# Optimization experiments

Hardware: AMD Instinct MI355X
Metric: run time of the kernel (lower is better)

Reference implementation:

```python
import jax, jax.numpy as jnp
import numpy as np

BS, NQ, NK = 4096, 21, 7   # batch, num_neg queries, 7 keys (weekdays)
E = 512                     # key_size == query_size
H = 512                     # hidden_size
NEG_INF = -1e9


def setup_inputs() -> dict:
    key = jax.random.key(0)
    ks = jax.random.split(key, 6)
    sq = 1.0 / np.sqrt(E)
    sh = 1.0 / np.sqrt(H)
    return {
        "queries": jax.random.normal(ks[0], (BS, NQ, E), jnp.float32),
        "keys": jax.random.normal(ks[1], (BS, NK, E), jnp.float32),
        "wq_w": jax.random.normal(ks[2], (H, E), jnp.float32) * sq,
        "wq_b": jnp.zeros((H,), jnp.float32),
        "wk_w": jax.random.normal(ks[3], (H, E), jnp.float32) * sq,
        "wk_b": jnp.zeros((H,), jnp.float32),
        "wv_w": jax.random.normal(ks[4], (1, H), jnp.float32) * sh,
        "wv_b": jnp.zeros((1,), jnp.float32),
        "cum_subs_masks": jax.random.randint(ks[5], (BS, 1, NK, 1), 0, 2).astype(jnp.int32),
        "num_neg": NQ,
    }


def reference(queries, keys, wq_w, wq_b, wk_w, wk_b, wv_w, wv_b, cum_subs_masks, num_neg):
    # dropout p=0.0 -> identity (as in eval / p=0)
    q = jnp.einsum('bqe,he->bqh', queries, wq_w) + wq_b          # (bs,21,H)
    k = jnp.einsum('bke,he->bkh', keys, wk_w) + wk_b             # (bs,7,H)
    # additive score: broadcast q over keys, k over queries
    t = jnp.tanh(q[:, :, None, :] + k[:, None, :, :])            # (bs,21,7,H)
    scores = jnp.einsum('bqkh,oh->bqko', t, wv_w) + wv_b         # (bs,21,7,1)
    scores = scores + cum_subs_masks.astype(scores.dtype) * NEG_INF
    attn_weights = jax.nn.softmax(scores, axis=-2)               # softmax over 7 keys
    # weighted sum of the RAW keys (the module multiplies by expanded `keys`)
    attn_out = jnp.einsum('bqk,bke->bqe', attn_weights[..., 0], keys)  # (bs,21,E)
    return (attn_out, attn_weights)
```

## Files before the change

kernel.cpp:

```cpp
#include <hip/hip_runtime.h>
#include <hip/hip_bf16.h>

#define BS_   4096
#define NQ_   21
#define NK_   7
#define E_    512
#define MQ_   (BS_*NQ_)
#define MK_   (BS_*NK_)
#define MT1_  (MQ_/128)
#define MT2_  (MK_/128)
#define SCALE_ 2.88539008177792681f

typedef __attribute__((ext_vector_type(8))) short bf16x8;
typedef __attribute__((ext_vector_type(4))) float f32x4;
typedef __attribute__((ext_vector_type(8))) unsigned short u16x8;

__device__ __forceinline__ unsigned int cvt_pk_bf16(float lo, float hi){
  unsigned int r;
  asm("v_cvt_pk_bf16_f32 %0, %1, %2" : "=v"(r) : "v"(lo), "v"(hi));
  return r;
}
__device__ __forceinline__ float bf2f(unsigned short h){
  return __builtin_bit_cast(float, (unsigned int)h << 16);
}
__device__ __forceinline__ void gload_lds16(const void* g, void* l){
  __builtin_amdgcn_global_load_lds(
      (const __attribute__((address_space(1))) unsigned int*)g,
      (__attribute__((address_space(3))) unsigned int*)l, 16, 0, 0);
}

__global__ __launch_bounds__(256) void cast_weights(
    const float* __restrict__ wq, const float* __restrict__ wk,
    unsigned int* __restrict__ oq, unsigned int* __restrict__ ok)
{
  int i = blockIdx.x * 256 + threadIdx.x;
  float4 a = ((const float4*)wq)[i];
  float4 b = ((const float4*)wk)[i];
  uint2 ua = { cvt_pk_bf16(a.x, a.y), cvt_pk_bf16(a.z, a.w) };
  uint2 ub = { cvt_pk_bf16(b.x, b.y), cvt_pk_bf16(b.z, b.w) };
  ((uint2*)oq)[i] = ua;
  ((uint2*)ok)[i] = ub;
}

__global__ __launch_bounds__(256, 4)
void gemm_proj(const float* __restrict__ Aq, const float* __restrict__ Ak,
               const unsigned short* __restrict__ Bq, const unsigned short* __restrict__ Bk,
               const float* __restrict__ bq, const float* __restrict__ bk,
               unsigned short* __restrict__ Cq, unsigned short* __restrict__ Ck)
{
  __shared__ char Asm[2][128 * 64];
  __shared__ char Bsm[2][128 * 64];

  const int tid  = threadIdx.x;
  const int lane = tid & 63;
  const int w    = tid >> 6;
  const int wr   = w >> 1, wc = w & 1;

  const int orig = (int)blockIdx.x;
  const int j    = orig >> 3;
  int       mt   = (j >> 2) * 8 + (orig & 7);
  const int nt   = j & 3;

  const float* A; const unsigned short* Bw; const float* bias; unsigned short* C;
  if (mt < MT1_){ A = Aq; Bw = Bq; bias = bq; C = Cq; }
  else          { A = Ak; Bw = Bk; bias = bk; C = Ck; mt -= MT1_; }

  const long m0 = (long)mt << 7;
  const int  n0 = nt << 7;
  const char* Abyte = (const char*)(A + m0 * E_);
  const char* Bbyte = (const char*)Bw;

  long asrc[4]; int adst[4];
#pragma unroll
  for (int i = 0; i < 4; ++i){
    const int c   = tid + i * 256;
    const int row = c >> 3;
    const int sl  = c & 7;
    asrc[i] = (long)row * (E_ * 4) + sl * 16;
    adst[i] = row * 64 + (((sl & 6) * 8) ^ (((row >> 1) & 3) << 4)) + (sl & 1) * 8;
  }
  long bsrc[2]; int bdst[2];
#pragma unroll
  for (int i = 0; i < 2; ++i){
    const int c   = tid + i * 256;
    const int row = c >> 2;
    const int sl  = c & 3;
    bsrc[i] = (long)(n0 + row) * (E_ * 2) + ((sl * 16) ^ (((row >> 1) & 3) << 4));
    bdst[i] = c * 16;
  }

  int aoff[4], boff[4];
#pragma unroll
  for (int m = 0; m < 4; ++m){
    const int r = wr * 64 + m * 16 + (lane & 15);
    aoff[m] = r * 64 + ((16 * (lane >> 4)) ^ (((r >> 1) & 3) << 4));
  }
#pragma unroll
  for (int n = 0; n < 4; ++n){
    const int r = wc * 64 + n * 16 + (lane & 15);
    boff[n] = r * 64 + ((16 * (lane >> 4)) ^ (((r >> 1) & 3) << 4));
  }

  f32x4 acc[4][4];
  const f32x4 z4 = {0.f, 0.f, 0.f, 0.f};
#pragma unroll
  for (int m = 0; m < 4; ++m)
#pragma unroll
    for (int n = 0; n < 4; ++n) acc[m][n] = z4;

  {
    float4 av[4];
#pragma unroll
    for (int i = 0; i < 4; ++i) av[i] = *(const float4*)(Abyte + asrc[i]);
#pragma unroll
    for (int i = 0; i < 2; ++i) gload_lds16(Bbyte + bsrc[i], Bsm[0] + bdst[i]);
#pragma unroll
    for (int i = 0; i < 4; ++i){
      uint2 u = { cvt_pk_bf16(av[i].x, av[i].y), cvt_pk_bf16(av[i].z, av[i].w) };
      *(uint2*)(Asm[0] + adst[i]) = u;
    }
  }
  __syncthreads();

#pragma unroll 2
  for (int t = 0; t < 16; ++t){
    const int buf = t & 1, nbuf = buf ^ 1;
    float4 av[4];
    if (t < 15){
      const long ka = (long)(t + 1) * 128;
      const long kb = (long)(t + 1) * 64;
#pragma unroll
      for (int i = 0; i < 4; ++i) av[i] = *(const float4*)(Abyte + asrc[i] + ka);
#pragma unroll
      for (int i = 0; i < 2; ++i) gload_lds16(Bbyte + bsrc[i] + kb, Bsm[nbuf] + bdst[i]);
    }
    bf16x8 af[4], bfr[4];
#pragma unroll
    for (int m = 0; m < 4; ++m) af[m]  = *(const bf16x8*)(Asm[buf] + aoff[m]);
#pragma unroll
    for (int n = 0; n < 4; ++n) bfr[n] = *(const bf16x8*)(Bsm[buf] + boff[n]);
#pragma unroll
    for (int m = 0; m < 4; ++m)
#pragma unroll
      for (int n = 0; n < 4; ++n)
        acc[m][n] = __builtin_amdgcn_mfma_f32_16x16x32_bf16(af[m], bfr[n], acc[m][n], 0, 0, 0);
    if (t < 15){
#pragma unroll
      for (int i = 0; i < 4; ++i){
        uint2 u = { cvt_pk_bf16(av[i].x, av[i].y), cvt_pk_bf16(av[i].z, av[i].w) };
        *(uint2*)(Asm[nbuf] + adst[i]) = u;
      }
    }
    __syncthreads();
  }

  const int ccol0 = n0 + wc * 64 + (lane & 15);
  float bvs[4];
#pragma unroll
  for (int n = 0; n < 4; ++n) bvs[n] = bias[ccol0 + n * 16] * SCALE_;
#pragma unroll
  for (int m = 0; m < 4; ++m){
    const long rbase = m0 + wr * 64 + m * 16 + (lane >> 4) * 4;
#pragma unroll
    for (int n = 0; n < 4; ++n){
      const long col = ccol0 + n * 16;
      float v0 = fmaf(acc[m][n][0], SCALE_, bvs[n]);
      float v1 = fmaf(acc[m][n][1], SCALE_, bvs[n]);
      float v2 = fmaf(acc[m][n][2], SCALE_, bvs[n]);
      float v3 = fmaf(acc[m][n][3], SCALE_, bvs[n]);
      unsigned int u01 = cvt_pk_bf16(v0, v1);
      unsigned int u23 = cvt_pk_bf16(v2, v3);
      C[(rbase + 0) * E_ + col] = (unsigned short)(u01 & 0xffffu);
      C[(rbase + 1) * E_ + col] = (unsigned short)(u01 >> 16);
      C[(rbase + 2) * E_ + col] = (unsigned short)(u23 & 0xffffu);
      C[(rbase + 3) * E_ + col] = (unsigned short)(u23 >> 16);
    }
  }
}

__global__ __launch_bounds__(256, 2)
void attn_fused(const unsigned short* __restrict__ qp,
                const unsigned short* __restrict__ kp,
                const float* __restrict__ keys,
                const float* __restrict__ wv, const float* __restrict__ wvb,
                const int* __restrict__ mask,
                float* __restrict__ out0, float* __restrict__ out1)
{
  const int lane = threadIdx.x & 63;
  const int b    = blockIdx.x * 4 + (threadIdx.x >> 6);

  float wvr[8];
  *(float4*)&wvr[0] = ((const float4*)wv)[lane * 2];
  *(float4*)&wvr[4] = ((const float4*)wv)[lane * 2 + 1];

  float kf[NK_][8];
#pragma unroll
  for (int k = 0; k < NK_; ++k){
    u16x8 u = *(const u16x8*)(kp + ((long)b * NK_ + k) * E_ + lane * 8);
#pragma unroll
    for (int j = 0; j < 8; ++j) kf[k][j] = bf2f((unsigned short)u[j]);
  }
  float kr[NK_][8];
#pragma unroll
  for (int k = 0; k < NK_; ++k){
    const float4* p = (const float4*)(keys + ((long)b * NK_ + k) * E_ + lane * 8);
    *(float4*)&kr[k][0] = p[0];
    *(float4*)&kr[k][4] = p[1];
  }

  float wsum = ((wvr[0] + wvr[1]) + (wvr[2] + wvr[3])) + ((wvr[4] + wvr[5]) + (wvr[6] + wvr[7]));
#pragma unroll
  for (int off = 32; off; off >>= 1) wsum += __shfl_xor(wsum, off, 64);

  const float vb = wvb[0];
  float base[NK_];
#pragma unroll
  for (int k = 0; k < NK_; ++k)
    base[k] = (wsum + vb) + (float)mask[b * NK_ + k] * (-1e9f);

  const unsigned short* qrow = qp + (long)b * NQ_ * E_ + lane * 8;
  u16x8 qv = *(const u16x8*)qrow;

  float4* o0 = (float4*)(out0 + (long)b * NQ_ * E_) + lane * 2;
  float*  o1 = out1 + (long)b * (NQ_ * NK_);

  for (int qi = 0; qi < NQ_; ++qi){
    u16x8 qn = qv;
    if (qi < NQ_ - 1) qn = *(const u16x8*)(qrow + (qi + 1) * E_);

    float qf[8];
#pragma unroll
    for (int j = 0; j < 8; ++j) qf[j] = bf2f((unsigned short)qv[j]);
    qv = qn;

    float acc[NK_];
#pragma unroll
    for (int k = 0; k < NK_; ++k){
      float a = 0.f;
#pragma unroll
      for (int j = 0; j < 8; ++j){
        float x = qf[j] + kf[k][j];
        float e = __builtin_amdgcn_exp2f(x);
        float r = __builtin_amdgcn_rcpf(e + 1.0f);
        a = fmaf(wvr[j], r, a);
      }
      acc[k] = a;
    }
#pragma unroll
    for (int k = 0; k < NK_; ++k){
      float a = acc[k];
#pragma unroll
      for (int off = 32; off; off >>= 1) a += __shfl_xor(a, off, 64);
      acc[k] = a;
    }
    float sc[NK_], mx = -3.4e38f;
#pragma unroll
    for (int k = 0; k < NK_; ++k){ sc[k] = fmaf(-2.f, acc[k], base[k]); mx = fmaxf(mx, sc[k]); }
    float sum = 0.f;
#pragma unroll
    for (int k = 0; k < NK_; ++k){ sc[k] = __expf(sc[k] - mx); sum += sc[k]; }
    const float inv = __builtin_amdgcn_rcpf(sum);
    float wgt[NK_];
#pragma unroll
    for (int k = 0; k < NK_; ++k) wgt[k] = sc[k] * inv;

    float wsel = wgt[0];
#pragma unroll
    for (int k = 1; k < NK_; ++k) wsel = (lane == k) ? wgt[k] : wsel;
    if (lane < NK_) o1[qi * NK_ + lane] = wsel;

    float4 lo = {0.f,0.f,0.f,0.f}, hi = {0.f,0.f,0.f,0.f};
#pragma unroll
    for (int k = 0; k < NK_; ++k){
      lo.x = fmaf(wgt[k], kr[k][0], lo.x);
      lo.y = fmaf(wgt[k], kr[k][1], lo.y);
      lo.z = fmaf(wgt[k], kr[k][2], lo.z);
      lo.w = fmaf(wgt[k], kr[k][3], lo.w);
      hi.x = fmaf(wgt[k], kr[k][4], hi.x);
      hi.y = fmaf(wgt[k], kr[k][5], hi.y);
      hi.z = fmaf(wgt[k], kr[k][6], hi.z);
      hi.w = fmaf(wgt[k], kr[k][7], hi.w);
    }
    o0[qi * 128 + 0] = lo;
    o0[qi * 128 + 1] = hi;
  }
}

extern "C" void kernel_launch(void* const* d_in, const int* in_sizes, int n_in,
                              void* d_out, int out_size, void* d_ws, size_t ws_size,
                              hipStream_t stream)
{
  const float* queries = (const float*)d_in[0];
  const float* keys    = (const float*)d_in[1];
  const float* wq_w    = (const float*)d_in[2];
  const float* wq_b    = (const float*)d_in[3];
  const float* wk_w    = (const float*)d_in[4];
  const float* wk_b    = (const float*)d_in[5];
  const float* wv_w    = (const float*)d_in[6];
  const float* wv_b    = (const float*)d_in[7];
  const int*   mask    = (const int*)d_in[8];
  (void)in_sizes; (void)n_in; (void)out_size; (void)ws_size;

  float* out0 = (float*)d_out;
  float* out1 = out0 + (long)MQ_ * E_;

  char* ws = (char*)d_ws;
  unsigned short* wqb = (unsigned short*)ws;
  unsigned short* wkb = (unsigned short*)(ws + 512 * 512 * 2);
  unsigned short* qb  = (unsigned short*)(ws + (1 << 20));
  unsigned short* kb  = qb + (size_t)MQ_ * E_;

  cast_weights<<<dim3(256), dim3(256), 0, stream>>>(wq_w, wk_w, (unsigned int*)wqb, (unsigned int*)wkb);
  gemm_proj<<<dim3((MT1_ + MT2_) * 4), dim3(256), 0, stream>>>(
      queries, keys, wqb, wkb, wq_b, wk_b, qb, kb);
  attn_fused<<<dim3(BS_ / 4), dim3(256), 0, stream>>>(qb, kb, keys, wv_w, wv_b, mask, out0, out1);
}
```

Before: 251.6 us.

## Triple-buffer projection GEMM with two-stage-ahead prefetch and explicit waitcnts

Rewrites the projection GEMM main loop from a double-buffered scheme to a three-buffer pipeline that keeps loads for two K-steps in flight. It uses hand-placed s_waitcnt and raw barriers so global loads overlap with MFMA work across iterations. The loop is fully unrolled and the occupancy hint in launch_bounds is dropped. The extra LDS (48KB) and the extra register-held A tile may lower occupancy, and the manual waitcnt counts are fragile if the compiler reorders memory ops.

```diff
diff --git a/kernel.cpp b/kernel.cpp
--- a/kernel.cpp
+++ b/kernel.cpp
@@ -42,14 +42,14 @@
   ((uint2*)ok)[i] = ub;
 }
 
-__global__ __launch_bounds__(256, 4)
+__global__ __launch_bounds__(256)
 void gemm_proj(const float* __restrict__ Aq, const float* __restrict__ Ak,
                const unsigned short* __restrict__ Bq, const unsigned short* __restrict__ Bk,
                const float* __restrict__ bq, const float* __restrict__ bk,
                unsigned short* __restrict__ Cq, unsigned short* __restrict__ Ck)
 {
-  __shared__ char Asm[2][128 * 64];
-  __shared__ char Bsm[2][128 * 64];
+  __shared__ char Asm[3][128 * 64];
+  __shared__ char Bsm[3][128 * 64];
 
   const int tid  = threadIdx.x;
   const int lane = tid & 63;
@@ -108,51 +108,74 @@
 #pragma unroll
     for (int n = 0; n < 4; ++n) acc[m][n] = z4;
 
+#define STAGE_LOADS(av, T) do { \
+  _Pragma("unroll") for (int i_ = 0; i_ < 4; ++i_) \
+    av[i_] = *(const float4*)(Abyte + asrc[i_] + (long)(T) * 128); \
+} while(0)
+
+#define STAGE_B(BUF, T) do { \
+  _Pragma("unroll") for (int i_ = 0; i_ < 2; ++i_) \
+    gload_lds16(Bbyte + bsrc[i_] + (long)(T) * 64, Bsm[BUF] + bdst[i_]); \
+} while(0)
+
+#define WRITE_A(BUF, av) do { \
+  _Pragma("unroll") for (int i_ = 0; i_ < 4; ++i_){ \
+    uint2 u_ = { cvt_pk_bf16(av[i_].x, av[i_].y), cvt_pk_bf16(av[i_].z, av[i_].w) }; \
+    *(uint2*)(Asm[BUF] + adst[i_]) = u_; \
+  } \
+} while(0)
+
+#define COMPUTE(BUF) do { \
+  bf16x8 af_[4], bfr_[4]; \
+  _Pragma("unroll") for (int m_ = 0; m_ < 4; ++m_) af_[m_]  = *(const bf16x8*)(Asm[BUF] + aoff[m_]); \
+  _Pragma("unroll") for (int n_ = 0; n_ < 4; ++n_) bfr_[n_] = *(const bf16x8*)(Bsm[BUF] + boff[n_]); \
+  _Pragma("unroll") for (int m_ = 0; m_ < 4; ++m_) \
+    _Pragma("unroll") for (int n_ = 0; n_ < 4; ++n_) \
+      acc[m_][n_] = __builtin_amdgcn_mfma_f32_16x16x32_bf16(af_[m_], bfr_[n_], acc[m_][n_], 0, 0, 0); \
+} while(0)
+
+#define BARRIER() do { \
+  asm volatile("" ::: "memory"); \
+  __builtin_amdgcn_s_barrier(); \
+  asm volatile("" ::: "memory"); \
+} while(0)
+
+  float4 avA[4], avB[4];
+
+  STAGE_LOADS(avA, 0);  STAGE_B(0, 0);
+  STAGE_LOADS(avB, 1);  STAGE_B(1, 1);
+  asm volatile("s_waitcnt vmcnt(6)" ::: "memory");
+  WRITE_A(0, avA);
+
+#pragma unroll
+  for (int t = 0; t < 14; ++t){
+    const int cur = t % 3, nx1 = (t + 1) % 3, nx2 = (t + 2) % 3;
+    asm volatile("s_waitcnt vmcnt(2)" ::: "memory");
+    if ((t & 1) == 0) WRITE_A(nx1, avB); else WRITE_A(nx1, avA);
+    asm volatile("s_waitcnt lgkmcnt(0)" ::: "memory");
+    BARRIER();
+    if ((t & 1) == 0) STAGE_LOADS(avA, t + 2); else STAGE_LOADS(avB, t + 2);
+    STAGE_B(nx2, t + 2);
+    COMPUTE(cur);
+  }
   {
-    float4 av[4];
-#pragma unroll
-    for (int i = 0; i < 4; ++i) av[i] = *(const float4*)(Abyte + asrc[i]);
-#pragma unroll
-    for (int i = 0; i < 2; ++i) gload_lds16(Bbyte + bsrc[i], Bsm[0] + bdst[i]);
-#pragma unroll
-    for (int i = 0; i < 4; ++i){
-      uint2 u = { cvt_pk_bf16(av[i].x, av[i].y), cvt_pk_bf16(av[i].z, av[i].w) };
-      *(uint2*)(Asm[0] + adst[i]) = u;
-    }
-  }
-  __syncthreads();
-
-#pragma unroll 2
-  for (int t = 0; t < 16; ++t){
-    const int buf = t & 1, nbuf = buf ^ 1;
-    float4 av[4];
-    if (t < 15){
-      const long ka = (long)(t + 1) * 128;
-      const long kb = (long)(t + 1) * 64;
-#pragma unroll
-      for (int i = 0; i < 4; ++i) av[i] = *(const float4*)(Abyte + asrc[i] + ka);
-#pragma unroll
-      for (int i = 0; i < 2; ++i) gload_lds16(Bbyte + bsrc[i] + kb, Bsm[nbuf] + bdst[i]);
-    }
-    bf16x8 af[4], bfr[4];
-#pragma unroll
-    for (int m = 0; m < 4; ++m) af[m]  = *(const bf16x8*)(Asm[buf] + aoff[m]);
-#pragma unroll
-    for (int n = 0; n < 4; ++n) bfr[n] = *(const bf16x8*)(Bsm[buf] + boff[n]);
-#pragma unroll
-    for (int m = 0; m < 4; ++m)
-#pragma unroll
-      for (int n = 0; n < 4; ++n)
-        acc[m][n] = __builtin_amdgcn_mfma_f32_16x16x32_bf16(af[m], bfr[n], acc[m][n], 0, 0, 0);
-    if (t < 15){
-#pragma unroll
-      for (int i = 0; i < 4; ++i){
-        uint2 u = { cvt_pk_bf16(av[i].x, av[i].y), cvt_pk_bf16(av[i].z, av[i].w) };
-        *(uint2*)(Asm[nbuf] + adst[i]) = u;
-      }
-    }
-    __syncthreads();
-  }
+    asm volatile("s_waitcnt vmcnt(2)" ::: "memory");
+    WRITE_A(0 , avB);
+    asm volatile("s_waitcnt lgkmcnt(0)" ::: "memory");
+    BARRIER();
+    COMPUTE(2 );
+  }
+  {
+    asm volatile("s_waitcnt vmcnt(0)" ::: "memory");
+    BARRIER();
+    COMPUTE(0 );
+  }
+
+#undef STAGE_LOADS
+#undef STAGE_B
+#undef WRITE_A
+#undef COMPUTE
+#undef BARRIER
 
   const int ccol0 = n0 + wc * 64 + (lane & 15);
   float bvs[4];
```

Result: no change. 249.0 us (-1.0%).
